# Performance work log

Measured on AMD Instinct MI355X. Metric: run time of the kernel, lower is better.

Reference implementation:

```python
import jax, jax.numpy as jnp
import numpy as np

D = 256      # model dim
H = 4        # heads
L = 6        # layers (shared weights)
N = 32768    # neuron dim; per-head hidden = N//H = 8192
VOCAB = 256
B, T = 2, 2048
EPS = 1e-5


def _ln(x):
    # LayerNorm over last dim, no affine (matches nn.LayerNorm(D, elementwise_affine=False))
    m = jnp.mean(x, axis=-1, keepdims=True)
    v = jnp.mean((x - m) ** 2, axis=-1, keepdims=True)
    return (x - m) * jax.lax.rsqrt(v + EPS)


def _rope(x):
    # x: [B, H, T, d]
    d = x.shape[-1]
    t = x.shape[-2]
    inv_freq = 1.0 / (10000.0 ** (jnp.arange(0, d, 2, dtype=jnp.float32) / d))
    freqs = jnp.arange(t, dtype=jnp.float32)[:, None] * inv_freq[None, :]  # [T, d/2]
    emb = jnp.concatenate([freqs, freqs], axis=-1)                          # [T, d]
    x1, x2 = x[..., : d // 2], x[..., d // 2 :]
    x_rot = jnp.concatenate([-x2, x1], axis=-1)
    return x * jnp.cos(emb) + x_rot * jnp.sin(emb)


def _linear_attn(q, k, v):
    # q,k: [B,H,T,n]; v: [B,T,D]. Raw (unnormalized) scores, STRICTLY causal mask
    # (tril with diagonal=-1, i.e. token t attends to s < t only), no softmax.
    qr = _rope(q)
    kr = _rope(k)
    scores = jnp.einsum('bhtn,bhsn->bhts', qr, kr)  # [B,H,T,T]
    t_idx = jnp.arange(q.shape[-2])
    mask = t_idx[:, None] > t_idx[None, :]          # strict lower triangle
    scores = jnp.where(mask, scores, jnp.zeros((), scores.dtype))
    return jnp.einsum('bhts,bsd->bhtd', scores, v)  # [B,H,T,D]


def setup_inputs() -> dict:
    key = jax.random.key(0)
    ks = jax.random.split(key, 6)
    idx = jax.random.randint(ks[0], (B, T), 0, VOCAB, dtype=jnp.int64)
    std = 0.02
    wte = std * jax.random.normal(ks[1], (VOCAB, D), dtype=jnp.float32)
    encoder = std * jax.random.normal(ks[2], (N, D), dtype=jnp.float32)
    decoder_x = std * jax.random.normal(ks[3], (H, D, N // H), dtype=jnp.float32)
    decoder_y = std * jax.random.normal(ks[4], (H, D, N // H), dtype=jnp.float32)
    readout = std * jax.random.normal(ks[5], (D, VOCAB), dtype=jnp.float32)
    return {"idx": idx, "wte": wte, "encoder": encoder,
            "decoder_x": decoder_x, "decoder_y": decoder_y, "readout": readout}


def reference(idx, wte, encoder, decoder_x, decoder_y, readout):
    # Dropout is identity in eval mode.
    v_ast = _ln(wte[idx])  # [B,T,D]
    for _ in range(L):  # weights SHARED across layers
        x = jax.nn.relu(jnp.einsum('btd,hdn->bhtn', v_ast, decoder_x))  # [B,H,T,N/H]
        a_ast = _linear_attn(x, x, v_ast)                               # [B,H,T,D]
        y = jax.nn.relu(jnp.einsum('bhtd,hdn->bhtn', _ln(a_ast), decoder_y)) * x
        y_flat = jnp.transpose(y, (0, 2, 1, 3)).reshape(y.shape[0], y.shape[2], N)  # [B,T,N]
        v_ast = _ln(v_ast + _ln(y_flat @ encoder))
    return v_ast @ readout  # [B,T,VOCAB]
```

## Files before the change

### kernel.cpp

```cpp
#include <hip/hip_runtime.h>
#include <stdint.h>

typedef unsigned short u16;
typedef __bf16 bfv8 __attribute__((ext_vector_type(8)));
typedef float f32x4 __attribute__((ext_vector_type(4)));

#define BM 128
#define BN 128
#define BK 32

__device__ __forceinline__ float b2f(u16 u){ union{float f; unsigned int i;} x; x.i = ((unsigned int)u)<<16; return x.f; }
__device__ __forceinline__ u16 f2b(float f){ union{float f; unsigned int i;} x; x.f = f; unsigned int r = x.i + 0x7fffu + ((x.i>>16)&1u); return (u16)(r>>16); }

__device__ __forceinline__ void load16_lds(const void* g, void* l){
  __builtin_amdgcn_global_load_lds(
      (const __attribute__((address_space(1))) void*)g,
      (__attribute__((address_space(3))) void*)l, 16, 0, 0);
}

__device__ __forceinline__ void swz(int& bx, int& by, int& bz){
  int gx = gridDim.x, gy = gridDim.y;
  int nw = gx*gy*gridDim.z;
  int flat = blockIdx.x + gx*(blockIdx.y + gy*blockIdx.z);
  int q = nw >> 3, r = nw & 7, xcd = flat & 7, i = flat >> 3;
  int wg = (xcd < r ? xcd*(q+1) : r*(q+1) + (xcd-r)*q) + i;
  bx = wg % gx; int t = wg / gx; by = t % gy; bz = t / gy;
}

struct GP {
  const u16* A; const u16* Bt; const u16* A2; const u16* Bt2;
  const u16* ct; const u16* st;
  float* Cf; u16* Cb; u16* Y;
  int bh0, zs, zm;
};

template<int LDA, int LDB, bool PAIRB>
__device__ __forceinline__ void kloop(const u16* A, const u16* Bt, int m0, int n0,
                                      int kbeg, int kend,
                                      u16 (&As)[2][4096], u16 (&Bs)[2][4096],
                                      f32x4 (&acc)[4][4]){
  const int tid = threadIdx.x;
  const int lane = tid & 63;
  const int wid = tid >> 6;
  const int wm = wid >> 1, wn = wid & 1;
  const int srow = tid >> 2, sslot = tid & 3;
  const int nt = (kend - kbeg) / BK;
  if (nt <= 0) return;

  auto stage = [&](int k0, int buf){
    #pragma unroll
    for (int q = 0; q < 2; ++q){
      int row = q*64 + srow;
      int ks = sslot ^ ((row >> 1) & 3);
      load16_lds(A + (long)(m0 + row)*LDA + (k0 + ks*8), &As[buf][q*2048 + wid*512]);
    }
    #pragma unroll
    for (int q = 0; q < 2; ++q){
      int row = q*64 + srow;
      int ks = sslot ^ ((row >> 1) & 3);
      long brow;
      if (PAIRB){ int wnb = row >> 6, sub = (row >> 5) & 1, r5 = row & 31;
                  brow = n0 + wnb*32 + r5 + sub*4096; }
      else brow = n0 + row;
      load16_lds(Bt + brow*(long)LDB + (k0 + ks*8), &Bs[buf][q*2048 + wid*512]);
    }
  };
  auto compute = [&](int buf){
    bfv8 af[4], bf[4];
    const int r16 = lane & 15, s4 = lane >> 4;
    #pragma unroll
    for (int i = 0; i < 4; ++i){
      int ar = wm*64 + i*16 + r16;
      af[i] = *(const bfv8*)(&As[buf][ar*BK + ((s4 ^ ((ar>>1)&3))*8)]);
      int br = wn*64 + i*16 + r16;
      bf[i] = *(const bfv8*)(&Bs[buf][br*BK + ((s4 ^ ((br>>1)&3))*8)]);
    }
    #pragma unroll
    for (int i = 0; i < 4; ++i)
      #pragma unroll
      for (int j = 0; j < 4; ++j)
        acc[i][j] = __builtin_amdgcn_mfma_f32_16x16x32_bf16(af[i], bf[j], acc[i][j], 0,0,0);
  };

  stage(kbeg, 0);
  int cur = 0;
  for (int t = 0; t < nt-1; ++t){
    stage(kbeg + (t+1)*BK, cur^1);
    asm volatile("s_waitcnt vmcnt(4)" ::: "memory");
    __builtin_amdgcn_s_barrier();
    compute(cur);
    asm volatile("s_waitcnt lgkmcnt(0)" ::: "memory");
    __builtin_amdgcn_s_barrier();
    cur ^= 1;
  }
  asm volatile("s_waitcnt vmcnt(0)" ::: "memory");
  __builtin_amdgcn_s_barrier();
  compute(cur);
  asm volatile("s_waitcnt lgkmcnt(0)" ::: "memory");
  __builtin_amdgcn_s_barrier();
}

#define EPI_SETUP const int lane = threadIdx.x & 63, wid = threadIdx.x >> 6; \
  const int wm = wid >> 1, wn = wid & 1; const int r16 = lane & 15, s4 = lane >> 4;

__global__ __launch_bounds__(256) void g_rope(GP p){
  int bx, by, bz; swz(bx, by, bz);
  const int m0 = by*BM, n0 = bx*64, z = bz;
  const int bh = p.bh0 + z, b = bh >> 2, h = bh & 3;
  __shared__ u16 As[2][4096], Bs[2][4096];
  f32x4 acc[4][4] = {};
  kloop<256,256,true>(p.A + (long)b*524288, p.Bt + (long)h*2097152, m0, n0, 0, 256, As, Bs, acc);
  EPI_SETUP
  #pragma unroll
  for (int i = 0; i < 4; ++i)
    #pragma unroll
    for (int j = 0; j < 2; ++j){
      int cl = n0 + wn*32 + j*16 + r16;
      #pragma unroll
      for (int v = 0; v < 4; ++v){
        int row = m0 + wm*64 + i*16 + s4*4 + v;
        float x1 = fmaxf(acc[i][j][v], 0.f);
        float x2 = fmaxf(acc[i][j+2][v], 0.f);
        float c = b2f(p.ct[(long)row*4096 + cl]);
        float s = b2f(p.st[(long)row*4096 + cl]);
        p.Cb[(long)z*16777216 + (long)row*8192 + cl]        = f2b(x1*c - x2*s);
        p.Cb[(long)z*16777216 + (long)row*8192 + cl + 4096] = f2b(x2*c + x1*s);
      }
    }
}

__global__ __launch_bounds__(256) void g_qk(GP p){
  int bx, by, bz; swz(bx, by, bz);
  const int m0 = by*BM, n0 = bx*BN, z = bz;
  if (n0 >= m0 + BM) return;
  __shared__ u16 As[2][4096], Bs[2][4096];
  f32x4 acc[4][4] = {};
  const u16* A = p.A + (long)z*16777216;
  kloop<8192,8192,false>(A, A, m0, n0, 0, 8192, As, Bs, acc);
  EPI_SETUP
  u16* C = p.Cb + (long)z*4194304;
  #pragma unroll
  for (int i = 0; i < 4; ++i)
    #pragma unroll
    for (int j = 0; j < 4; ++j){
      int col = n0 + wn*64 + j*16 + r16;
      #pragma unroll
      for (int v = 0; v < 4; ++v){
        int row = m0 + wm*64 + i*16 + s4*4 + v;
        C[(long)row*2048 + col] = f2b(row > col ? acc[i][j][v] : 0.f);
      }
    }
}

__global__ __launch_bounds__(256) void g_pv(GP p){
  int bx, by, bz; swz(bx, by, bz);
  const int m0 = by*BM, n0 = bx*BN;
  const int head = bz >> p.zs, sl = bz & p.zm;
  const int b = (p.bh0 + head) >> 2;
  const int kc = 2048 >> p.zs;
  const int kbeg = sl*kc;
  const int kend = min(min(2048, m0 + BM), kbeg + kc);
  __shared__ u16 As[2][4096], Bs[2][4096];
  f32x4 acc[4][4] = {};
  kloop<2048,2048,false>(p.A + (long)head*4194304, p.Bt + (long)b*524288, m0, n0, kbeg, kend, As, Bs, acc);
  EPI_SETUP
  #pragma unroll
  for (int i = 0; i < 4; ++i)
    #pragma unroll
    for (int j = 0; j < 4; ++j){
      int col = n0 + wn*64 + j*16 + r16;
      #pragma unroll
      for (int v = 0; v < 4; ++v){
        int row = m0 + wm*64 + i*16 + s4*4 + v;
        p.Cf[(long)bz*524288 + (long)row*256 + col] = acc[i][j][v];
      }
    }
}

__global__ __launch_bounds__(256) void g_fuse(GP p){
  int bx, by, bz; swz(bx, by, bz);
  const int m0 = by*BM, n0 = bx*BN, z = bz;
  const int bh = p.bh0 + z, b = bh >> 2, h = bh & 3;
  __shared__ u16 As[2][4096], Bs[2][4096];
  f32x4 acc1[4][4] = {}, acc2[4][4] = {};
  kloop<256,256,false>(p.A  + (long)z*524288, p.Bt  + (long)h*2097152, m0, n0, 0, 256, As, Bs, acc1);
  kloop<256,256,false>(p.A2 + (long)b*524288, p.Bt2 + (long)h*2097152, m0, n0, 0, 256, As, Bs, acc2);
  EPI_SETUP
  #pragma unroll
  for (int i = 0; i < 4; ++i)
    #pragma unroll
    for (int j = 0; j < 4; ++j){
      int col = n0 + wn*64 + j*16 + r16;
      #pragma unroll
      for (int v = 0; v < 4; ++v){
        int row = m0 + wm*64 + i*16 + s4*4 + v;
        p.Y[(long)z*16777216 + (long)row*8192 + col] =
            f2b(fmaxf(acc1[i][j][v], 0.f) * fmaxf(acc2[i][j][v], 0.f));
      }
    }
}

__global__ __launch_bounds__(256) void g_enc(GP p){
  int bx, by, bz; swz(bx, by, bz);
  const int m0 = by*BM, n0 = bx*BN;
  const int head = bz >> p.zs, sp = bz & p.zm;
  const int h = (p.bh0 + head) & 3;
  const int kc = 8192 >> p.zs;
  const int kbeg = sp*kc, kend = kbeg + kc;
  __shared__ u16 As[2][4096], Bs[2][4096];
  f32x4 acc[4][4] = {};
  kloop<8192,32768,false>(p.A + (long)head*16777216, p.Bt + (long)h*8192, m0, n0, kbeg, kend, As, Bs, acc);
  EPI_SETUP
  #pragma unroll
  for (int i = 0; i < 4; ++i)
    #pragma unroll
    for (int j = 0; j < 4; ++j){
      int col = n0 + wn*64 + j*16 + r16;
      #pragma unroll
      for (int v = 0; v < 4; ++v){
        int row = m0 + wm*64 + i*16 + s4*4 + v;
        p.Cf[(long)bz*524288 + (long)row*256 + col] = acc[i][j][v];
      }
    }
}

__global__ __launch_bounds__(256) void g_out(GP p){
  int bx, by, bz; swz(bx, by, bz); (void)bz;
  const int m0 = by*BM, n0 = bx*BN;
  __shared__ u16 As[2][4096], Bs[2][4096];
  f32x4 acc[4][4] = {};
  kloop<256,256,false>(p.A, p.Bt, m0, n0, 0, 256, As, Bs, acc);
  EPI_SETUP
  #pragma unroll
  for (int i = 0; i < 4; ++i)
    #pragma unroll
    for (int j = 0; j < 4; ++j){
      int col = n0 + wn*64 + j*16 + r16;
      #pragma unroll
      for (int v = 0; v < 4; ++v){
        int row = m0 + wm*64 + i*16 + s4*4 + v;
        p.Cf[(long)row*256 + col] = acc[i][j][v];
      }
    }
}


__device__ __forceinline__ float wave_sum(float v){
  #pragma unroll
  for (int o = 32; o > 0; o >>= 1) v += __shfl_down(v, o, 64);
  return v;
}
__device__ __forceinline__ float block_sum(float v, float* sm){
  v = wave_sum(v);
  __syncthreads();
  if ((threadIdx.x & 63) == 0) sm[threadIdx.x >> 6] = v;
  __syncthreads();
  return sm[0] + sm[1] + sm[2] + sm[3];
}

__global__ __launch_bounds__(256) void k_embed(const int* idx, const float* wte,
                                               u16* vbf, u16* vbt){
  __shared__ float sm[4];
  __shared__ int is64_s;
  int row = blockIdx.x, d = threadIdx.x;
  int oddnz = (d < 64) ? (idx[2*d + 1] != 0) : 0;
  unsigned long long mb = __ballot(oddnz);
  if (threadIdx.x == 0) is64_s = (mb == 0ULL);
  __syncthreads();
  int tok = is64_s ? idx[2*row] : idx[row];
  float x = wte[tok*256 + d];
  float m = block_sum(x, sm) * (1.f/256.f);
  float dd = x - m;
  float var = block_sum(dd*dd, sm) * (1.f/256.f);
  float y = dd * rsqrtf(var + 1e-5f);
  vbf[(long)row*256 + d] = f2b(y);
  int b = row >> 11, t = row & 2047;
  vbt[((long)(b*256 + d))*2048 + t] = f2b(y);
}

__global__ __launch_bounds__(256) void k_ln(const float* abuf, u16* out, int pv){
  __shared__ float sm[4];
  int row = blockIdx.x, d = threadIdx.x;
  int head = row >> 11, t = row & 2047;
  float x = 0.f;
  for (int s = 0; s < pv; ++s) x += abuf[((long)(head*pv + s) << 19) + (long)t*256 + d];
  float m = block_sum(x, sm) * (1.f/256.f);
  float dd = x - m;
  float var = block_sum(dd*dd, sm) * (1.f/256.f);
  out[(long)row*256 + d] = f2b(dd * rsqrtf(var + 1e-5f));
}

__global__ __launch_bounds__(256) void k_acc(const float* part, float* t1,
                                             int bh0, int gc, int ps){
  int t = blockIdx.x, d = threadIdx.x;
  long o = (long)t*256 + d;
  float s0 = 0.f, s1 = 0.f;
  for (int z = 0; z < gc; ++z){
    float v = 0.f;
    for (int sp = 0; sp < ps; ++sp) v += part[((long)(z*ps + sp) << 19) + o];
    if (((bh0 + z) >> 2) == 0) s0 += v; else s1 += v;
  }
  #pragma unroll
  for (int b = 0; b < 2; ++b){
    int lo = bh0 > 4*b ? bh0 : 4*b;
    int hi = (bh0 + gc) < (4*b + 4) ? (bh0 + gc) : (4*b + 4);
    if (lo < hi){
      float s = b == 0 ? s0 : s1;
      if (lo == 4*b) t1[((long)b << 19) + o] = s;
      else           t1[((long)b << 19) + o] += s;
    }
  }
}

__global__ __launch_bounds__(256) void k_finish(const float* t1, u16* vbf, u16* vbt){
  __shared__ float sm[4];
  int row = blockIdx.x; int d = threadIdx.x;
  int b = row >> 11, t = row & 2047;
  float s = t1[(long)row*256 + d];
  float m = block_sum(s, sm) * (1.f/256.f);
  float dd = s - m;
  float var = block_sum(dd*dd, sm) * (1.f/256.f);
  float u = dd * rsqrtf(var + 1e-5f);
  float wv = b2f(vbf[(long)row*256 + d]) + u;
  float m2 = block_sum(wv, sm) * (1.f/256.f);
  float d2 = wv - m2;
  float v2 = block_sum(d2*d2, sm) * (1.f/256.f);
  float y = d2 * rsqrtf(v2 + 1e-5f);
  vbf[(long)row*256 + d] = f2b(y);
  vbt[((long)(b*256 + d))*2048 + t] = f2b(y);
}

__global__ __launch_bounds__(256) void k_cossin(u16* ct, u16* st){
  int tid = blockIdx.x*256 + threadIdx.x;
  int t = tid >> 12, i = tid & 4095;
  float f = powf(10000.0f, -(float)i * (1.0f/4096.0f));
  float a = (float)t * f;
  float s, c; sincosf(a, &s, &c);
  ct[tid] = f2b(c); st[tid] = f2b(s);
}

__global__ void k_transpose(const float* in, u16* out, int R, int C, long in_z, long out_z){
  __shared__ float tile[32][33];
  const float* I = in + (long)blockIdx.z * in_z;
  u16* O = out + (long)blockIdx.z * out_z;
  int c0 = blockIdx.x*32, r0 = blockIdx.y*32;
  int tx = threadIdx.x, ty = threadIdx.y;
  #pragma unroll
  for (int k = 0; k < 4; ++k){ int r = ty + k*8; tile[r][tx] = I[(long)(r0+r)*C + c0+tx]; }
  __syncthreads();
  #pragma unroll
  for (int k = 0; k < 4; ++k){ int r = ty + k*8; O[(long)(c0+r)*R + r0+tx] = f2b(tile[tx][r]); }
}


extern "C" void kernel_launch(void* const* d_in, const int* in_sizes, int n_in,
                              void* d_out, int out_size, void* d_ws, size_t ws_size,
                              hipStream_t stream){
  const int*   idx = (const int*)d_in[0];
  const float* wte = (const float*)d_in[1];
  const float* enc = (const float*)d_in[2];
  const float* dx  = (const float*)d_in[3];
  const float* dy  = (const float*)d_in[4];
  const float* ro  = (const float*)d_in[5];
  float* out = (float*)d_out;
  (void)in_sizes; (void)n_in; (void)out_size;

  int gc = 1, pv = 2;
  {
    const int gcs[4] = {4, 3, 2, 1};
    for (int i = 0; i < 4; ++i){
      int g = gcs[i]; int pvt = (g >= 4) ? 1 : 2;
      size_t need = 92274688UL + (size_t)g*(33554432UL + 8388608UL + (size_t)pvt*2097152UL);
      if (need <= ws_size){ gc = g; pv = pvt; break; }
    }
  }
  const int ps = 2;
  const int pvs = (pv == 2) ? 1 : 0;

  char* w = (char*)d_ws;
  size_t off = 0;
  auto alloc = [&](size_t b){ size_t r = off; off += (b + 255) & ~(size_t)255; return r; };
  u16*   v_bf  = (u16*)  (w + alloc(4096UL*256*2));
  u16*   v_bt  = (u16*)  (w + alloc(2UL*256*2048*2));
  u16*   dxT   = (u16*)  (w + alloc(4UL*8192*256*2));
  u16*   dyT   = (u16*)  (w + alloc(4UL*8192*256*2));
  u16*   encT  = (u16*)  (w + alloc(256UL*32768*2));
  u16*   ct    = (u16*)  (w + alloc(2048UL*4096*2));
  u16*   st    = (u16*)  (w + alloc(2048UL*4096*2));
  float* t1    = (float*)(w + alloc(2UL*2048*256*4));
  u16*   xbuf  = (u16*)  (w + alloc((size_t)gc*33554432));
  u16*   scb   = (u16*)  (w + alloc((size_t)gc*8388608));
  float* abuf  = (float*)(w + alloc((size_t)gc*pv*2097152UL));
  float* part  = (float*)scb;
  u16*   lnAb  = (u16*)((char*)scb + (size_t)gc*ps*2097152UL);
  u16*   roT   = (u16*)t1;

  dim3 tb(32, 8);
  k_cossin<<<32768, 256, 0, stream>>>(ct, st);
  k_transpose<<<dim3(256, 8, 4),  tb, 0, stream>>>(dx,  dxT,  256,   8192, 256L*8192, 8192L*256);
  k_transpose<<<dim3(256, 8, 4),  tb, 0, stream>>>(dy,  dyT,  256,   8192, 256L*8192, 8192L*256);
  k_transpose<<<dim3(8, 1024, 1), tb, 0, stream>>>(enc, encT, 32768, 256,  0, 0);
  k_embed<<<4096, 256, 0, stream>>>(idx, wte, v_bf, v_bt);

  for (int l = 0; l < 6; ++l){
    for (int bh0 = 0; bh0 < 8; bh0 += gc){
      int ze = (8 - bh0 < gc) ? (8 - bh0) : gc;
      { GP g{}; g.bh0=bh0; g.A=v_bf; g.Bt=dxT; g.ct=ct; g.st=st; g.Cb=xbuf;
        g_rope<<<dim3(64,16,ze), 256, 0, stream>>>(g); }
      { GP g{}; g.bh0=bh0; g.A=xbuf; g.Cb=scb;
        g_qk<<<dim3(16,16,ze), 256, 0, stream>>>(g); }
      { GP g{}; g.bh0=bh0; g.A=scb; g.Bt=v_bt; g.Cf=abuf; g.zs=pvs; g.zm=pv-1;
        g_pv<<<dim3(2,16,ze*pv), 256, 0, stream>>>(g); }
      k_ln<<<ze*2048, 256, 0, stream>>>(abuf, lnAb, pv);
      { GP g{}; g.bh0=bh0; g.A=lnAb; g.Bt=dyT; g.A2=v_bf; g.Bt2=dxT; g.Y=xbuf;
        g_fuse<<<dim3(64,16,ze), 256, 0, stream>>>(g); }
      { GP g{}; g.bh0=bh0; g.A=xbuf; g.Bt=encT; g.Cf=part; g.zs=1; g.zm=1;
        g_enc<<<dim3(2,16,ze*ps), 256, 0, stream>>>(g); }
      k_acc<<<2048, 256, 0, stream>>>(part, t1, bh0, ze, ps);
    }
    k_finish<<<4096, 256, 0, stream>>>(t1, v_bf, v_bt);
  }
  k_transpose<<<dim3(8, 8, 1), tb, 0, stream>>>(ro, roT, 256, 256, 0, 0);
  { GP g{}; g.A=v_bf; g.Bt=roT; g.Cf=out;
    g_out<<<dim3(2,32,1), 256, 0, stream>>>(g); }
}
```

Before: 8.165 ms.

## Use 256x256 tiles with 512-thread blocks for rope, qk and encoder GEMMs

Adds a kloop256 mainloop that computes 256x256 output tiles with 8 waves, each wave holding an 8x4 grid of MFMA accumulators. g_rope, g_qk and g_enc move to this larger tile and 512-thread blocks. The larger tile doubles operand reuse per LDS load and cuts global traffic for the big K=8192 GEMMs. In exchange it raises register pressure, doubles shared memory per block and leaves fewer blocks in the grid, which may reduce occupancy and the number of active CUs. The causal skip in qk also becomes coarser.

```diff
diff --git a/kernel.cpp b/kernel.cpp
--- a/kernel.cpp
+++ b/kernel.cpp
@@ -100,25 +100,98 @@
   __builtin_amdgcn_s_barrier();
 }
 
+template<int LDA, int LDB, int PAIR>
+__device__ __forceinline__ void kloop256(const u16* A, const u16* Bt, int m0, int n0,
+                                         int kbeg, int kend,
+                                         u16 (&As)[2][8192], u16 (&Bs)[2][8192],
+                                         f32x4 (&acc)[8][4]){
+  const int tid = threadIdx.x;
+  const int lane = tid & 63;
+  const int wid = tid >> 6;
+  const int srow = tid >> 2;
+  const int sslot = tid & 3;
+  const int nt = (kend - kbeg) / BK;
+  if (nt <= 0) return;
+
+  auto stage = [&](int k0, int buf){
+    #pragma unroll
+    for (int q = 0; q < 2; ++q){
+      int row = q*128 + srow;
+      int ks = sslot ^ ((row >> 1) & 3);
+      load16_lds(A + (long)(m0 + row)*LDA + (k0 + ks*8), &As[buf][q*4096 + wid*512]);
+    }
+    #pragma unroll
+    for (int q = 0; q < 2; ++q){
+      int row = q*128 + srow;
+      int ks = sslot ^ ((row >> 1) & 3);
+      long brow;
+      if (PAIR) brow = n0 + (row & 127) + (long)(row >> 7)*4096;
+      else      brow = n0 + row;
+      load16_lds(Bt + brow*(long)LDB + (k0 + ks*8), &Bs[buf][q*4096 + wid*512]);
+    }
+  };
+  auto compute = [&](int buf){
+    const int wm = wid >> 2, wn = wid & 3;
+    const int r16 = lane & 15, s4 = lane >> 4;
+    bfv8 af[8], bf[4];
+    #pragma unroll
+    for (int i = 0; i < 8; ++i){
+      int ar = wm*128 + i*16 + r16;
+      af[i] = *(const bfv8*)(&As[buf][ar*BK + ((s4 ^ ((ar>>1)&3))*8)]);
+    }
+    #pragma unroll
+    for (int j = 0; j < 4; ++j){
+      int br;
+      if (PAIR) br = (j < 2) ? (wn*32 + j*16 + r16) : (128 + wn*32 + (j-2)*16 + r16);
+      else      br = wn*64 + j*16 + r16;
+      bf[j] = *(const bfv8*)(&Bs[buf][br*BK + ((s4 ^ ((br>>1)&3))*8)]);
+    }
+    #pragma unroll
+    for (int i = 0; i < 8; ++i)
+      #pragma unroll
+      for (int j = 0; j < 4; ++j)
+        acc[i][j] = __builtin_amdgcn_mfma_f32_16x16x32_bf16(af[i], bf[j], acc[i][j], 0,0,0);
+  };
+
+  stage(kbeg, 0);
+  int cur = 0;
+  for (int t = 0; t < nt-1; ++t){
+    stage(kbeg + (t+1)*BK, cur^1);
+    asm volatile("s_waitcnt vmcnt(4)" ::: "memory");
+    __builtin_amdgcn_s_barrier();
+    compute(cur);
+    asm volatile("s_waitcnt lgkmcnt(0)" ::: "memory");
+    __builtin_amdgcn_s_barrier();
+    cur ^= 1;
+  }
+  asm volatile("s_waitcnt vmcnt(0)" ::: "memory");
+  __builtin_amdgcn_s_barrier();
+  compute(cur);
+  asm volatile("s_waitcnt lgkmcnt(0)" ::: "memory");
+  __builtin_amdgcn_s_barrier();
+}
+
 #define EPI_SETUP const int lane = threadIdx.x & 63, wid = threadIdx.x >> 6; \
   const int wm = wid >> 1, wn = wid & 1; const int r16 = lane & 15, s4 = lane >> 4;
-
-__global__ __launch_bounds__(256) void g_rope(GP p){
+#define EPI_SETUP8 const int lane = threadIdx.x & 63, wid = threadIdx.x >> 6; \
+  const int wm = wid >> 2, wn = wid & 3; const int r16 = lane & 15, s4 = lane >> 4;
+
+__global__ __launch_bounds__(512) void g_rope(GP p){
   int bx, by, bz; swz(bx, by, bz);
-  const int m0 = by*BM, n0 = bx*64, z = bz;
+  const int m0 = by*256, n0 = bx*128, z = bz;
   const int bh = p.bh0 + z, b = bh >> 2, h = bh & 3;
-  __shared__ u16 As[2][4096], Bs[2][4096];
-  f32x4 acc[4][4] = {};
-  kloop<256,256,true>(p.A + (long)b*524288, p.Bt + (long)h*2097152, m0, n0, 0, 256, As, Bs, acc);
-  EPI_SETUP
-  #pragma unroll
-  for (int i = 0; i < 4; ++i)
+  __shared__ u16 As[2][8192], Bs[2][8192];
+  f32x4 acc[8][4] = {};
+  kloop256<256,256,1>(p.A + (long)b*524288, p.Bt + (long)h*2097152, m0, n0, 0, 256, As, Bs, acc);
+  EPI_SETUP8
+  #pragma unroll
+  for (int i = 0; i < 8; ++i)
     #pragma unroll
     for (int j = 0; j < 2; ++j){
       int cl = n0 + wn*32 + j*16 + r16;
       #pragma unroll
       for (int v = 0; v < 4; ++v){
-        int row = m0 + wm*64 + i*16 + s4*4 + v;
+        int row = m0 + wm*128 + i*16 + s4*4 + v;
         float x1 = fmaxf(acc[i][j][v], 0.f);
         float x2 = fmaxf(acc[i][j+2][v], 0.f);
         float c = b2f(p.ct[(long)row*4096 + cl]);
@@ -129,25 +202,48 @@
     }
 }
 
-__global__ __launch_bounds__(256) void g_qk(GP p){
+__global__ __launch_bounds__(512) void g_qk(GP p){
   int bx, by, bz; swz(bx, by, bz);
-  const int m0 = by*BM, n0 = bx*BN, z = bz;
-  if (n0 >= m0 + BM) return;
-  __shared__ u16 As[2][4096], Bs[2][4096];
-  f32x4 acc[4][4] = {};
+  const int m0 = by*256, n0 = bx*256, z = bz;
+  if (n0 > m0) return;
+  __shared__ u16 As[2][8192], Bs[2][8192];
+  f32x4 acc[8][4] = {};
   const u16* A = p.A + (long)z*16777216;
-  kloop<8192,8192,false>(A, A, m0, n0, 0, 8192, As, Bs, acc);
-  EPI_SETUP
+  kloop256<8192,8192,0>(A, A, m0, n0, 0, 8192, As, Bs, acc);
+  EPI_SETUP8
   u16* C = p.Cb + (long)z*4194304;
   #pragma unroll
-  for (int i = 0; i < 4; ++i)
+  for (int i = 0; i < 8; ++i)
     #pragma unroll
     for (int j = 0; j < 4; ++j){
       int col = n0 + wn*64 + j*16 + r16;
       #pragma unroll
       for (int v = 0; v < 4; ++v){
-        int row = m0 + wm*64 + i*16 + s4*4 + v;
+        int row = m0 + wm*128 + i*16 + s4*4 + v;
         C[(long)row*2048 + col] = f2b(row > col ? acc[i][j][v] : 0.f);
+      }
+    }
+}
+
+__global__ __launch_bounds__(512) void g_enc(GP p){
+  int bx, by, bz; swz(bx, by, bz);
+  const int m0 = by*256, sp = bx, head = bz;
+  const int h = (p.bh0 + head) & 3;
+  const int kbeg = sp*4096, kend = kbeg + 4096;
+  __shared__ u16 As[2][8192], Bs[2][8192];
+  f32x4 acc[8][4] = {};
+  kloop256<8192,32768,0>(p.A + (long)head*16777216, p.Bt + (long)h*8192, m0, 0, kbeg, kend, As, Bs, acc);
+  EPI_SETUP8
+  float* C = p.Cf + (long)(head*2 + sp)*524288;
+  #pragma unroll
+  for (int i = 0; i < 8; ++i)
+    #pragma unroll
+    for (int j = 0; j < 4; ++j){
+      int col = wn*64 + j*16 + r16;
+      #pragma unroll
+      for (int v = 0; v < 4; ++v){
+        int row = m0 + wm*128 + i*16 + s4*4 + v;
+        C[(long)row*256 + col] = acc[i][j][v];
       }
     }
 }
@@ -196,30 +292,6 @@
         int row = m0 + wm*64 + i*16 + s4*4 + v;
         p.Y[(long)z*16777216 + (long)row*8192 + col] =
             f2b(fmaxf(acc1[i][j][v], 0.f) * fmaxf(acc2[i][j][v], 0.f));
-      }
-    }
-}
-
-__global__ __launch_bounds__(256) void g_enc(GP p){
-  int bx, by, bz; swz(bx, by, bz);
-  const int m0 = by*BM, n0 = bx*BN;
-  const int head = bz >> p.zs, sp = bz & p.zm;
-  const int h = (p.bh0 + head) & 3;
-  const int kc = 8192 >> p.zs;
-  const int kbeg = sp*kc, kend = kbeg + kc;
-  __shared__ u16 As[2][4096], Bs[2][4096];
-  f32x4 acc[4][4] = {};
-  kloop<8192,32768,false>(p.A + (long)head*16777216, p.Bt + (long)h*8192, m0, n0, kbeg, kend, As, Bs, acc);
-  EPI_SETUP
-  #pragma unroll
-  for (int i = 0; i < 4; ++i)
-    #pragma unroll
-    for (int j = 0; j < 4; ++j){
-      int col = n0 + wn*64 + j*16 + r16;
-      #pragma unroll
-      for (int v = 0; v < 4; ++v){
-        int row = m0 + wm*64 + i*16 + s4*4 + v;
-        p.Cf[(long)bz*524288 + (long)row*256 + col] = acc[i][j][v];
       }
     }
 }
@@ -406,16 +478,16 @@
     for (int bh0 = 0; bh0 < 8; bh0 += gc){
       int ze = (8 - bh0 < gc) ? (8 - bh0) : gc;
       { GP g{}; g.bh0=bh0; g.A=v_bf; g.Bt=dxT; g.ct=ct; g.st=st; g.Cb=xbuf;
-        g_rope<<<dim3(64,16,ze), 256, 0, stream>>>(g); }
+        g_rope<<<dim3(32,8,ze), 512, 0, stream>>>(g); }
       { GP g{}; g.bh0=bh0; g.A=xbuf; g.Cb=scb;
-        g_qk<<<dim3(16,16,ze), 256, 0, stream>>>(g); }
+        g_qk<<<dim3(8,8,ze), 512, 0, stream>>>(g); }
       { GP g{}; g.bh0=bh0; g.A=scb; g.Bt=v_bt; g.Cf=abuf; g.zs=pvs; g.zm=pv-1;
         g_pv<<<dim3(2,16,ze*pv), 256, 0, stream>>>(g); }
       k_ln<<<ze*2048, 256, 0, stream>>>(abuf, lnAb, pv);
       { GP g{}; g.bh0=bh0; g.A=lnAb; g.Bt=dyT; g.A2=v_bf; g.Bt2=dxT; g.Y=xbuf;
         g_fuse<<<dim3(64,16,ze), 256, 0, stream>>>(g); }
-      { GP g{}; g.bh0=bh0; g.A=xbuf; g.Bt=encT; g.Cf=part; g.zs=1; g.zm=1;
-        g_enc<<<dim3(2,16,ze*ps), 256, 0, stream>>>(g); }
+      { GP g{}; g.bh0=bh0; g.A=xbuf; g.Bt=encT; g.Cf=part;
+        g_enc<<<dim3(ps,8,ze), 512, 0, stream>>>(g); }
       k_acc<<<2048, 256, 0, stream>>>(part, t1, bh0, ze, ps);
     }
     k_finish<<<4096, 256, 0, stream>>>(t1, v_bf, v_bt);
```

After: 8.809 ms. 7.9% more time.
